# Performance work log

Measured on AMD Instinct MI355X. Metric: run time of the kernel, lower is better.

The kernel has to match this reference:

```python
import jax, jax.numpy as jnp
import numpy as np

TEMPERATURE = 0.07
BASE_TEMPERATURE = 1.0
CONF_EMA_M = 0.99


def setup_inputs() -> dict:
    key = jax.random.key(0)
    k1, k2, k3 = jax.random.split(key, 3)
    b, n, q, k = 64, 30000, 32, 100
    return {
        "output": jax.random.normal(k1, (b, b, q, k), dtype=jnp.float32),
        "confidence": jax.random.uniform(k2, (n, q, k), dtype=jnp.float32),
        "batch_index": jax.random.randint(k3, (b,), 0, n, dtype=jnp.int64 if jax.config.read('jax_enable_x64') else jnp.int32),
        "x_mask": jnp.ones((b, q, k), dtype=bool),
        "topk": 3,
    }


def reference(output, confidence, batch_index, x_mask, topk):
    b, _, q, k = output.shape
    # output / T, rearrange 'b1 b2 q k -> b1 q (b2 k)', log-softmax over (b2 k)
    x = output / TEMPERATURE
    x = jnp.transpose(x, (0, 2, 1, 3)).reshape(b, q, b * k)
    x = jax.nn.log_softmax(x, axis=-1)
    atten = jnp.transpose(x.reshape(b, q, b, k), (0, 2, 1, 3))  # [b1,b2,q,k]
    logit = jnp.einsum('iiqk->iqk', atten)  # diagonal over (b1,b2) -> [b,q,k]

    # pseudo target from confidence buffer, masked
    pseudo = jnp.where(x_mask, confidence[batch_index], 0.0)
    # top-k mask along region axis (no-grad in original)
    kk = min(int(topk), k)
    _, idx = jax.lax.top_k(pseudo, kk)  # [b,q,kk]
    bi = jnp.arange(b)[:, None, None]
    qi = jnp.arange(q)[None, :, None]
    tmask = jnp.zeros(pseudo.shape, dtype=bool).at[bi, qi, idx].set(True)
    mask = tmask & x_mask
    pseudo = jnp.where(mask, pseudo, 0.0)
    phrase_mask = mask[:, :, 0]

    eps = jnp.finfo(logit.dtype).eps
    loss = -(pseudo * logit).sum(-1)
    loss = loss.sum() / (phrase_mask.sum() + eps)
    loss = loss * BASE_TEMPERATURE

    # confidence score (no-grad branch): masked softmax over regions
    neg_inf = jnp.finfo(logit.dtype).max
    logit_m = jnp.where(x_mask, logit, -neg_inf)  # in-place masked_fill_ in torch
    conf = jax.nn.softmax(logit_m, axis=-1)
    conf = jnp.where(x_mask, conf, 0.0)

    # hard EMA scatter update of confidence buffer
    hard = jax.nn.one_hot(jnp.argmax(conf, axis=-1), k, dtype=confidence.dtype)
    hard = jnp.where(x_mask, hard, 0.0)
    new_confidence = confidence.at[batch_index].set(
        CONF_EMA_M * confidence[batch_index] + (1.0 - CONF_EMA_M) * hard
    )
    return loss, atten, logit_m, pseudo, conf, new_confidence
```

## Files before the change

kernel.cpp:

```cpp
#include <hip/hip_runtime.h>
#include <float.h>
#include <math.h>

#define Bdim 64
#define Qdim 32
#define Kdim 100
#define QK   (Qdim*Kdim)
#define ROWLEN (Bdim*Kdim)
#define EPT  (ROWLEN/256)

__device__ inline float wred_max(float v){ for(int o=32;o;o>>=1) v=fmaxf(v,__shfl_down(v,o)); return v; }
__device__ inline float wred_sum(float v){ for(int o=32;o;o>>=1) v+=__shfl_down(v,o); return v; }

__global__ __launch_bounds__(256) void conloss_main(
    const float* __restrict__ out_in, const float* __restrict__ conf_in,
    const int* __restrict__ bidx, const int* __restrict__ xmask,
    const int* __restrict__ topk_p,
    float* __restrict__ atten_o, float* __restrict__ logitm_o,
    float* __restrict__ pseudo_o, float* __restrict__ conf_o,
    float* __restrict__ acc, int* __restrict__ hard_o)
{
    const int blk = blockIdx.x;
    const int i   = blk >> 5;
    const int qq  = blk & 31;
    const int tid = threadIdx.x;
    const size_t base = (size_t)i*(Bdim*QK) + (size_t)qq*Kdim;

    float vals[EPT];
    float lmax = -INFINITY;
    #pragma unroll
    for (int c = 0; c < EPT; ++c) {
        int e = tid + c*256;
        int j = e / Kdim, kk = e - j*Kdim;
        float v = out_in[base + (size_t)j*QK + kk] * (1.0f/0.07f);
        vals[c] = v;
        lmax = fmaxf(lmax, v);
    }
    __shared__ float red[4];
    __shared__ float s_max, s_lse;
    const int wid = tid >> 6, lane = tid & 63;
    float wm = wred_max(lmax);
    if (lane == 0) red[wid] = wm;
    __syncthreads();
    if (tid == 0) s_max = fmaxf(fmaxf(red[0],red[1]), fmaxf(red[2],red[3]));
    __syncthreads();
    const float m = s_max;
    float ls = 0.f;
    #pragma unroll
    for (int c = 0; c < EPT; ++c) ls += expf(vals[c] - m);
    float wsum = wred_sum(ls);
    if (lane == 0) red[wid] = wsum;
    __syncthreads();
    if (tid == 0) s_lse = m + logf(red[0]+red[1]+red[2]+red[3]);
    __syncthreads();
    const float lse = s_lse;

    __shared__ float sm_logit[Kdim];
    #pragma unroll
    for (int c = 0; c < EPT; ++c) {
        int e = tid + c*256;
        int j = e / Kdim, kk = e - j*Kdim;
        float a = vals[c] - lse;
        atten_o[base + (size_t)j*QK + kk] = a;
        if (j == i) sm_logit[kk] = a;
    }
    __syncthreads();

    __shared__ float sm_pseudo[Kdim], sm_lm[Kdim];
    __shared__ float s_cm, s_cs;
    __shared__ unsigned long long s_sel[2];
    const size_t ro = (size_t)i*QK + (size_t)qq*Kdim;
    const int row = bidx[i];
    if (tid < Kdim) {
        int kk = tid;
        bool xm = xmask[ro + kk] != 0;
        float pr = xm ? conf_in[(size_t)row*QK + (size_t)qq*Kdim + kk] : 0.0f;
        sm_pseudo[kk] = pr;
        float lm = xm ? sm_logit[kk] : -FLT_MAX;
        sm_lm[kk] = lm;
        logitm_o[ro + kk] = lm;
    }
    __syncthreads();
    if (tid == 0) {
        float cm = -FLT_MAX;
        for (int kk = 0; kk < Kdim; ++kk) cm = fmaxf(cm, sm_lm[kk]);
        float cs = 0.f;
        for (int kk = 0; kk < Kdim; ++kk) cs += expf(sm_lm[kk] - cm);
        s_cm = cm; s_cs = cs;
        int kt = *topk_p; if (kt > Kdim) kt = Kdim;
        unsigned long long sel0 = 0ull, sel1 = 0ull;
        for (int t = 0; t < kt; ++t) {
            float bv = -INFINITY; int bsel = -1;
            for (int kk = 0; kk < Kdim; ++kk) {
                bool taken = (kk < 64) ? ((sel0 >> kk) & 1ull) : ((sel1 >> (kk-64)) & 1ull);
                if (!taken && sm_pseudo[kk] > bv) { bv = sm_pseudo[kk]; bsel = kk; }
            }
            if (bsel >= 0) { if (bsel < 64) sel0 |= 1ull<<bsel; else sel1 |= 1ull<<(bsel-64); }
        }
        s_sel[0] = sel0; s_sel[1] = sel1;
        float lsum = 0.f;
        for (int kk = 0; kk < Kdim; ++kk) {
            bool selb = (kk<64) ? ((sel0>>kk)&1ull) : ((sel1>>(kk-64))&1ull);
            if (selb) lsum += sm_pseudo[kk] * sm_logit[kk];
        }
        atomicAdd(&acc[0], lsum);
        bool phrase = ((sel0 & 1ull) != 0) && (xmask[ro] != 0);
        if (phrase) atomicAdd(&acc[1], 1.0f);
        float bv = -1.f; int barg = 0;
        for (int kk = 0; kk < Kdim; ++kk) {
            bool xm = xmask[ro+kk] != 0;
            float cv = xm ? expf(sm_lm[kk]-cm)/cs : 0.f;
            if (cv > bv) { bv = cv; barg = kk; }
        }
        hard_o[i*Qdim + qq] = barg;
    }
    __syncthreads();
    if (tid < Kdim) {
        int kk = tid;
        bool xm = xmask[ro+kk] != 0;
        float cv = xm ? expf(sm_lm[kk]-s_cm)/s_cs : 0.f;
        conf_o[ro+kk] = cv;
        bool selb = (kk<64) ? ((s_sel[0]>>kk)&1ull) : ((s_sel[1]>>(kk-64))&1ull);
        pseudo_o[ro+kk] = selb ? sm_pseudo[kk] : 0.f;
    }
}

__global__ __launch_bounds__(256) void conloss_copy(
    const float* __restrict__ src, float* __restrict__ dst, long long n)
{
    long long idx = (long long)blockIdx.x*blockDim.x + threadIdx.x;
    const long long stride = (long long)gridDim.x*blockDim.x;
    for (; idx + 3*stride < n; idx += 4*stride) {
        float a = src[idx];
        float b = src[idx +   stride];
        float c = src[idx + 2*stride];
        float d = src[idx + 3*stride];
        dst[idx]            = a;
        dst[idx +   stride] = b;
        dst[idx + 2*stride] = c;
        dst[idx + 3*stride] = d;
    }
    for (; idx < n; idx += stride) dst[idx] = src[idx];
}

__global__ __launch_bounds__(256) void conloss_ema(
    const float* __restrict__ conf_in, const int* __restrict__ bidx,
    const int* __restrict__ xmask, const int* __restrict__ hard,
    float* __restrict__ newconf_o)
{
    const int i = blockIdx.x;
    const int row = bidx[i];
    for (int ii = i+1; ii < Bdim; ++ii) if (bidx[ii] == row) return;
    for (int e = threadIdx.x; e < QK; e += blockDim.x) {
        int qq = e / Kdim, kk = e - qq*Kdim;
        bool xm = xmask[(size_t)i*QK + e] != 0;
        float h = (xm && kk == hard[i*Qdim + qq]) ? 1.0f : 0.0f;
        newconf_o[(size_t)row*QK + e] = 0.99f*conf_in[(size_t)row*QK + e] + 0.01f*h;
    }
}

__global__ void conloss_final(const float* __restrict__ acc, float* __restrict__ loss_o)
{
    loss_o[0] = -acc[0] / (acc[1] + 1.1920929e-07f);
}

extern "C" void kernel_launch(void* const* d_in, const int* in_sizes, int n_in,
                              void* d_out, int out_size, void* d_ws, size_t ws_size,
                              hipStream_t stream) {
    const float* out_in  = (const float*)d_in[0];
    const float* conf_in = (const float*)d_in[1];
    const int*   bidx    = (const int*)d_in[2];
    const int*   xmask   = (const int*)d_in[3];
    const int*   topk    = (const int*)d_in[4];

    float* o = (float*)d_out;
    float* loss_o   = o;
    float* atten_o  = o + 1;
    float* logitm_o = atten_o + (size_t)Bdim*Bdim*Qdim*Kdim;
    float* pseudo_o = logitm_o + (size_t)Bdim*Qdim*Kdim;
    float* conf_o   = pseudo_o + (size_t)Bdim*Qdim*Kdim;
    float* newconf_o= conf_o   + (size_t)Bdim*Qdim*Kdim;

    float* acc  = (float*)d_ws;
    int*   hard = (int*)((char*)d_ws + 64);

    const long long nconf = (long long)in_sizes[1];

    hipMemsetAsync(d_ws, 0, 64, stream);
    conloss_main<<<Bdim*Qdim, 256, 0, stream>>>(out_in, conf_in, bidx, xmask, topk,
                                                atten_o, logitm_o, pseudo_o, conf_o,
                                                acc, hard);
    conloss_copy<<<16384, 256, 0, stream>>>(conf_in, newconf_o, nconf);
    conloss_ema<<<Bdim, 256, 0, stream>>>(conf_in, bidx, xmask, hard, newconf_o);
    conloss_final<<<1, 1, 0, stream>>>(acc, loss_o);
}
```

Baseline: 894.3 us.

## Fuse confidence copy into main kernel, vectorize loads, and parallelize top-k/argmax

Merges the confidence-buffer copy into the main softmax kernel as extra blocks, so both run concurrently in one launch. Switches the log-softmax row loads to float4 and uses nontemporal stores for the large atten output and the copy. Replaces the single-thread serial top-k, argmax and softmax reductions with wavefront shuffle reductions, and folds the final loss computation into the EMA kernel to drop one launch. The copy path assumes an offset of 3 floats for 16-byte alignment of the output, and the atten stores stay scalar, so vector store efficiency may be limited.

```diff
diff --git a/kernel.cpp b/kernel.cpp
--- a/kernel.cpp
+++ b/kernel.cpp
@@ -7,34 +7,71 @@
 #define Kdim 100
 #define QK   (Qdim*Kdim)
 #define ROWLEN (Bdim*Kdim)
-#define EPT  (ROWLEN/256)
+#define ROWV  (ROWLEN/4)
+#define MAIN_BLOCKS (Bdim*Qdim)
+#define COPY_BLOCKS 16384
+
+typedef float floatx4 __attribute__((ext_vector_type(4)));
 
 __device__ inline float wred_max(float v){ for(int o=32;o;o>>=1) v=fmaxf(v,__shfl_down(v,o)); return v; }
 __device__ inline float wred_sum(float v){ for(int o=32;o;o>>=1) v+=__shfl_down(v,o); return v; }
 
-__global__ __launch_bounds__(256) void conloss_main(
+__global__ __launch_bounds__(256) void conloss_fused(
     const float* __restrict__ out_in, const float* __restrict__ conf_in,
     const int* __restrict__ bidx, const int* __restrict__ xmask,
     const int* __restrict__ topk_p,
     float* __restrict__ atten_o, float* __restrict__ logitm_o,
     float* __restrict__ pseudo_o, float* __restrict__ conf_o,
+    float* __restrict__ newconf_o, long long nconf,
     float* __restrict__ acc, int* __restrict__ hard_o)
 {
+    const int tid = threadIdx.x;
+
+    if (blockIdx.x >= MAIN_BLOCKS) {
+        const long long nv = (nconf - 3) >> 2;
+        const float* __restrict__ s = conf_in + 3;
+        float*       __restrict__ d = newconf_o + 3;
+        long long v = (long long)(blockIdx.x - MAIN_BLOCKS)*256 + tid;
+        const long long str = (long long)(gridDim.x - MAIN_BLOCKS)*256;
+        for (; v < nv; v += str) {
+            const long long b = v << 2;
+            floatx4 t;
+            t.x = __builtin_nontemporal_load(s + b);
+            t.y = __builtin_nontemporal_load(s + b + 1);
+            t.z = __builtin_nontemporal_load(s + b + 2);
+            t.w = __builtin_nontemporal_load(s + b + 3);
+            __builtin_nontemporal_store(t, (floatx4*)(d + b));
+        }
+        if (blockIdx.x == MAIN_BLOCKS) {
+            if (tid < 3) newconf_o[tid] = conf_in[tid];
+            const long long tb = 3 + (nv << 2);
+            const int tcnt = (int)(nconf - tb);
+            if (tid >= 3 && tid < 3 + tcnt) {
+                const long long ix = tb + (tid - 3);
+                newconf_o[ix] = conf_in[ix];
+            }
+        }
+        return;
+    }
+
     const int blk = blockIdx.x;
     const int i   = blk >> 5;
     const int qq  = blk & 31;
-    const int tid = threadIdx.x;
-    const size_t base = (size_t)i*(Bdim*QK) + (size_t)qq*Kdim;
-
-    float vals[EPT];
+    const int base_v = i*(Bdim*QK/4) + qq*(Kdim/4);
+    const floatx4* __restrict__ out4 = (const floatx4*)out_in;
+
+    floatx4 vv[7];
     float lmax = -INFINITY;
     #pragma unroll
-    for (int c = 0; c < EPT; ++c) {
-        int e = tid + c*256;
-        int j = e / Kdim, kk = e - j*Kdim;
-        float v = out_in[base + (size_t)j*QK + kk] * (1.0f/0.07f);
-        vals[c] = v;
-        lmax = fmaxf(lmax, v);
+    for (int c = 0; c < 7; ++c) {
+        if (c < 6 || tid < 64) {
+            int ve = tid + c*256;
+            int j = ve/25, k4 = ve - j*25;
+            floatx4 v = out4[base_v + j*(QK/4) + k4];
+            v *= (1.0f/0.07f);
+            vv[c] = v;
+            lmax = fmaxf(lmax, fmaxf(fmaxf(v.x, v.y), fmaxf(v.z, v.w)));
+        }
     }
     __shared__ float red[4];
     __shared__ float s_max, s_lse;
@@ -47,7 +84,12 @@
     const float m = s_max;
     float ls = 0.f;
     #pragma unroll
-    for (int c = 0; c < EPT; ++c) ls += expf(vals[c] - m);
+    for (int c = 0; c < 7; ++c) {
+        if (c < 6 || tid < 64) {
+            floatx4 v = vv[c];
+            ls += expf(v.x-m) + expf(v.y-m) + expf(v.z-m) + expf(v.w-m);
+        }
+    }
     float wsum = wred_sum(ls);
     if (lane == 0) red[wid] = wsum;
     __syncthreads();
@@ -55,14 +97,21 @@
     __syncthreads();
     const float lse = s_lse;
 
-    __shared__ float sm_logit[Kdim];
+    __shared__ __align__(16) float sm_logit[Kdim];
+    const size_t fbase = (size_t)i*(Bdim*QK) + (size_t)qq*Kdim;
     #pragma unroll
-    for (int c = 0; c < EPT; ++c) {
-        int e = tid + c*256;
-        int j = e / Kdim, kk = e - j*Kdim;
-        float a = vals[c] - lse;
-        atten_o[base + (size_t)j*QK + kk] = a;
-        if (j == i) sm_logit[kk] = a;
+    for (int c = 0; c < 7; ++c) {
+        if (c < 6 || tid < 64) {
+            int ve = tid + c*256;
+            int j = ve/25, k4 = ve - j*25;
+            floatx4 a = vv[c] - lse;
+            float* ap = atten_o + fbase + (size_t)j*QK + 4*k4;
+            __builtin_nontemporal_store(a.x, ap);
+            __builtin_nontemporal_store(a.y, ap+1);
+            __builtin_nontemporal_store(a.z, ap+2);
+            __builtin_nontemporal_store(a.w, ap+3);
+            if (j == i) *(floatx4*)&sm_logit[4*k4] = a;
+        }
     }
     __syncthreads();
 
@@ -81,74 +130,72 @@
         logitm_o[ro + kk] = lm;
     }
     __syncthreads();
-    if (tid == 0) {
-        float cm = -FLT_MAX;
-        for (int kk = 0; kk < Kdim; ++kk) cm = fmaxf(cm, sm_lm[kk]);
-        float cs = 0.f;
-        for (int kk = 0; kk < Kdim; ++kk) cs += expf(sm_lm[kk] - cm);
-        s_cm = cm; s_cs = cs;
+    if (tid < 64) {
+        const bool has2 = (tid + 64) < Kdim;
+        float l0 = sm_lm[tid];
+        float l1 = has2 ? sm_lm[tid+64] : -FLT_MAX;
+        float cmv = wred_max(fmaxf(l0, l1));
+        cmv = __shfl(cmv, 0);
+        float es = expf(l0 - cmv) + (has2 ? expf(l1 - cmv) : 0.f);
+        float csv = wred_sum(es);
+        csv = __shfl(csv, 0);
+        if (tid == 0) { s_cm = cmv; s_cs = csv; }
+        float av = l0; int ai = tid;
+        if (has2 && l1 > av) { av = l1; ai = tid + 64; }
+        for (int o = 32; o; o >>= 1) {
+            float ov = __shfl_down(av, o); int oi = __shfl_down(ai, o);
+            if (ov > av || (ov == av && oi < ai)) { av = ov; ai = oi; }
+        }
+        if (tid == 0) hard_o[i*Qdim + qq] = ai;
+        float p0 = sm_pseudo[tid];
+        float p1 = has2 ? sm_pseudo[tid+64] : -INFINITY;
         int kt = *topk_p; if (kt > Kdim) kt = Kdim;
         unsigned long long sel0 = 0ull, sel1 = 0ull;
+        float lsum = 0.f;
         for (int t = 0; t < kt; ++t) {
-            float bv = -INFINITY; int bsel = -1;
-            for (int kk = 0; kk < Kdim; ++kk) {
-                bool taken = (kk < 64) ? ((sel0 >> kk) & 1ull) : ((sel1 >> (kk-64)) & 1ull);
-                if (!taken && sm_pseudo[kk] > bv) { bv = sm_pseudo[kk]; bsel = kk; }
+            float rv = p0; int ri = tid;
+            if (p1 > rv) { rv = p1; ri = tid + 64; }
+            for (int o = 32; o; o >>= 1) {
+                float ov = __shfl_down(rv, o); int oi = __shfl_down(ri, o);
+                if (ov > rv || (ov == rv && oi < ri)) { rv = ov; ri = oi; }
             }
-            if (bsel >= 0) { if (bsel < 64) sel0 |= 1ull<<bsel; else sel1 |= 1ull<<(bsel-64); }
-        }
-        s_sel[0] = sel0; s_sel[1] = sel1;
-        float lsum = 0.f;
-        for (int kk = 0; kk < Kdim; ++kk) {
-            bool selb = (kk<64) ? ((sel0>>kk)&1ull) : ((sel1>>(kk-64))&1ull);
-            if (selb) lsum += sm_pseudo[kk] * sm_logit[kk];
-        }
-        atomicAdd(&acc[0], lsum);
-        bool phrase = ((sel0 & 1ull) != 0) && (xmask[ro] != 0);
-        if (phrase) atomicAdd(&acc[1], 1.0f);
-        float bv = -1.f; int barg = 0;
-        for (int kk = 0; kk < Kdim; ++kk) {
-            bool xm = xmask[ro+kk] != 0;
-            float cv = xm ? expf(sm_lm[kk]-cm)/cs : 0.f;
-            if (cv > bv) { bv = cv; barg = kk; }
-        }
-        hard_o[i*Qdim + qq] = barg;
+            const int w = __shfl(ri, 0);
+            if (w == tid) p0 = -INFINITY;
+            if (has2 && w == tid + 64) p1 = -INFINITY;
+            if (tid == 0) {
+                if (w < 64) sel0 |= 1ull << w; else sel1 |= 1ull << (w - 64);
+                lsum += rv * sm_logit[w];
+            }
+        }
+        if (tid == 0) {
+            s_sel[0] = sel0; s_sel[1] = sel1;
+            atomicAdd(&acc[0], lsum);
+            if (((sel0 & 1ull) != 0) && (xmask[ro] != 0)) atomicAdd(&acc[1], 1.0f);
+        }
     }
     __syncthreads();
     if (tid < Kdim) {
         int kk = tid;
-        bool xm = xmask[ro+kk] != 0;
-        float cv = xm ? expf(sm_lm[kk]-s_cm)/s_cs : 0.f;
-        conf_o[ro+kk] = cv;
-        bool selb = (kk<64) ? ((s_sel[0]>>kk)&1ull) : ((s_sel[1]>>(kk-64))&1ull);
-        pseudo_o[ro+kk] = selb ? sm_pseudo[kk] : 0.f;
+        bool xm = xmask[ro + kk] != 0;
+        float cv = xm ? expf(sm_lm[kk] - s_cm) / s_cs : 0.f;
+        conf_o[ro + kk] = cv;
+        bool selb = (kk < 64) ? ((s_sel[0] >> kk) & 1ull) : ((s_sel[1] >> (kk-64)) & 1ull);
+        pseudo_o[ro + kk] = selb ? sm_pseudo[kk] : 0.f;
     }
 }
 
-__global__ __launch_bounds__(256) void conloss_copy(
-    const float* __restrict__ src, float* __restrict__ dst, long long n)
-{
-    long long idx = (long long)blockIdx.x*blockDim.x + threadIdx.x;
-    const long long stride = (long long)gridDim.x*blockDim.x;
-    for (; idx + 3*stride < n; idx += 4*stride) {
-        float a = src[idx];
-        float b = src[idx +   stride];
-        float c = src[idx + 2*stride];
-        float d = src[idx + 3*stride];
-        dst[idx]            = a;
-        dst[idx +   stride] = b;
-        dst[idx + 2*stride] = c;
-        dst[idx + 3*stride] = d;
-    }
-    for (; idx < n; idx += stride) dst[idx] = src[idx];
-}
-
-__global__ __launch_bounds__(256) void conloss_ema(
+__global__ __launch_bounds__(256) void conloss_tail(
     const float* __restrict__ conf_in, const int* __restrict__ bidx,
     const int* __restrict__ xmask, const int* __restrict__ hard,
-    float* __restrict__ newconf_o)
+    float* __restrict__ newconf_o, const float* __restrict__ acc,
+    float* __restrict__ loss_o)
 {
     const int i = blockIdx.x;
+    if (i == Bdim) {
+        if (threadIdx.x == 0)
+            loss_o[0] = -acc[0] / (acc[1] + 1.1920929e-07f);
+        return;
+    }
     const int row = bidx[i];
     for (int ii = i+1; ii < Bdim; ++ii) if (bidx[ii] == row) return;
     for (int e = threadIdx.x; e < QK; e += blockDim.x) {
@@ -157,11 +204,6 @@
         float h = (xm && kk == hard[i*Qdim + qq]) ? 1.0f : 0.0f;
         newconf_o[(size_t)row*QK + e] = 0.99f*conf_in[(size_t)row*QK + e] + 0.01f*h;
     }
-}
-
-__global__ void conloss_final(const float* __restrict__ acc, float* __restrict__ loss_o)
-{
-    loss_o[0] = -acc[0] / (acc[1] + 1.1920929e-07f);
 }
 
 extern "C" void kernel_launch(void* const* d_in, const int* in_sizes, int n_in,
@@ -187,10 +229,10 @@
     const long long nconf = (long long)in_sizes[1];
 
     hipMemsetAsync(d_ws, 0, 64, stream);
-    conloss_main<<<Bdim*Qdim, 256, 0, stream>>>(out_in, conf_in, bidx, xmask, topk,
-                                                atten_o, logitm_o, pseudo_o, conf_o,
-                                                acc, hard);
-    conloss_copy<<<16384, 256, 0, stream>>>(conf_in, newconf_o, nconf);
-    conloss_ema<<<Bdim, 256, 0, stream>>>(conf_in, bidx, xmask, hard, newconf_o);
-    conloss_final<<<1, 1, 0, stream>>>(acc, loss_o);
+    conloss_fused<<<MAIN_BLOCKS + COPY_BLOCKS, 256, 0, stream>>>(
+        out_in, conf_in, bidx, xmask, topk,
+        atten_o, logitm_o, pseudo_o, conf_o,
+        newconf_o, nconf, acc, hard);
+    conloss_tail<<<Bdim + 1, 256, 0, stream>>>(conf_in, bidx, xmask, hard,
+                                               newconf_o, acc, loss_o);
 }
```

New measurement: 736.6 us. 1.21x faster.
